# Kernel tuning notes

Measured on AMD Instinct MI355X. Metric: run time of the kernel, lower is better.

## Reference

```python
import jax, jax.numpy as jnp
import numpy as np

N, E, D, G, NTYPES = 50000, 400000, 64, 512, 64


def _bn(x, g, b):
    # BatchNorm1d in training mode: biased batch stats, eps=1e-5, affine g/b
    mu = x.mean(0)
    var = ((x - mu) ** 2).mean(0)
    return g * (x - mu) * jax.lax.rsqrt(var + 1e-5) + b


def _rotmat(a):
    t, p, q = a[0], a[1], a[2]
    ct, st = jnp.cos(t), jnp.sin(t)
    cp, sp = jnp.cos(p), jnp.sin(p)
    cq, sq = jnp.cos(q), jnp.sin(q)
    z = jnp.zeros(())
    o = jnp.ones(())
    Rt = jnp.array([[ct, -st, z], [st, ct, z], [z, z, o]])
    Rp = jnp.array([[cp, z, -sp], [z, o, z], [sp, z, cp]])
    Rq = jnp.array([[o, z, z], [z, cq, -sq], [z, sq, cq]])
    return Rt @ Rp @ Rq


def _egat(src, dst, nf, ef, Wnode, bnode, Wni, Wnj, Wfij, attn, H):
    # DGL EGATConv: edge feats from src/dst node + edge projections, edge-softmax attention over dst
    n = nf.shape[0]
    f_out = jax.nn.leaky_relu((nf @ Wni)[src] + (nf @ Wnj)[dst] + ef @ Wfij)  # [E, H*D]
    f_out = f_out.reshape(-1, H, D)
    e = (f_out * attn[None]).sum(-1)  # [E, H]
    emax = jax.ops.segment_max(e, dst, num_segments=n)
    ee = jnp.exp(e - emax[dst])
    a = ee / jax.ops.segment_sum(ee, dst, num_segments=n)[dst]
    hsrc = (nf @ Wnode + bnode).reshape(n, H, D)[src]
    h_out = jax.ops.segment_sum(hsrc * a[:, :, None], dst, num_segments=n)  # [N, H, D]
    return h_out, f_out


def _layer(src, dst, nh, eh, p, H, last):
    Wnode, bnode, Wni, Wnj, Wfij, attn, bnn_g, bnn_b, bne_g, bne_b, Wpn, bpn, Wpe, bpe = p
    hn, he = _egat(src, dst, nh, eh, Wnode, bnode, Wni, Wnj, Wfij, attn, H)
    if last:
        hn, he = hn.mean(1), he.mean(1)
    else:
        hn, he = hn.reshape(hn.shape[0], -1), he.reshape(he.shape[0], -1)
    hn = _bn(hn, bnn_g, bnn_b)
    he = _bn(he, bne_g, bne_b)
    return hn @ Wpn + bpn + nh, he @ Wpe + bpe + eh


def setup_inputs():
    key = jax.random.key(0)
    kit = iter(jax.random.split(key, 64))

    def rn(shape, s=0.05):
        return jax.random.normal(next(kit), shape, dtype=jnp.float32) * s

    inp = {}
    inp["ntype"] = jax.random.randint(next(kit), (N, 1), 0, NTYPES)
    inp["src"] = jax.random.randint(next(kit), (E,), 0, N)
    inp["dst"] = jax.random.randint(next(kit), (E,), 0, N)
    inp["graph_ids"] = jnp.sort(jax.random.randint(next(kit), (N,), 0, G))
    inp["angles_rot"] = rn((3,), 1.0)
    inp["angles_ref"] = rn((3,), 1.0)
    inp["efeats"] = rn((E, 3), 1.0)
    inp["emb_table"] = rn((NTYPES, D))
    inp["enc_W"] = rn((D, D)); inp["enc_b"] = jnp.zeros((D,))
    inp["ee_W1"] = rn((3, D)); inp["ee_b1"] = jnp.zeros((D,))
    inp["ee_W2"] = rn((D, D)); inp["ee_b2"] = jnp.zeros((D,))
    for nm in ["enc_bn1", "enc_bn2", "ee_bn1", "ee_bn2"]:
        inp[nm + "_g"] = jnp.ones((D,)); inp[nm + "_b"] = jnp.zeros((D,))
    for l, H in [(0, 2), (1, 1)]:
        p = "l%d_" % l
        inp[p + "Wnode"] = rn((D, H * D)); inp[p + "bnode"] = jnp.zeros((H * D,))
        inp[p + "Wni"] = rn((D, H * D)); inp[p + "Wnj"] = rn((D, H * D)); inp[p + "Wfij"] = rn((D, H * D))
        inp[p + "attn"] = rn((H, D))
        inp[p + "bnn_g"] = jnp.ones((H * D,)); inp[p + "bnn_b"] = jnp.zeros((H * D,))
        inp[p + "bne_g"] = jnp.ones((H * D,)); inp[p + "bne_b"] = jnp.zeros((H * D,))
        inp[p + "Wpn"] = rn((H * D, D)); inp[p + "bpn"] = jnp.zeros((D,))
        inp[p + "Wpe"] = rn((H * D, D)); inp[p + "bpe"] = jnp.zeros((D,))
    inp["dec_W"] = rn((4, D, D)); inp["dec_b"] = jnp.zeros((4, D))
    inp["dec_bn_g"] = jnp.ones((4, D)); inp["dec_bn_b"] = jnp.zeros((4, D))
    inp["dec_prelu"] = jnp.full((4,), 0.25, dtype=jnp.float32)
    inp["dec_Wout"] = rn((D, 1)); inp["dec_bout"] = jnp.zeros((1,))
    return inp


def reference(efeats, emb_table, enc_bn1_g, enc_bn1_b, enc_W, enc_b, enc_bn2_g, enc_bn2_b, ee_W1, ee_b1, ee_bn1_g, ee_bn1_b, ee_W2, ee_b2, ee_bn2_g, ee_bn2_b, l0_Wnode, l0_bnode, l0_Wni, l0_Wnj, l0_Wfij, l0_attn, l0_bnn_g, l0_bnn_b, l0_bne_g, l0_bne_b, l0_Wpn, l0_bpn, l0_Wpe, l0_bpe, l1_Wnode, l1_bnode, l1_Wni, l1_Wnj, l1_Wfij, l1_attn, l1_bnn_g, l1_bnn_b, l1_bne_g, l1_bne_b, l1_Wpn, l1_bpn, l1_Wpe, l1_bpe, dec_W, dec_b, dec_bn_g, dec_bn_b, dec_prelu, dec_Wout, dec_bout, ntype, src, dst, graph_ids, angles_rot, angles_ref):
    # node encoder: Embedding -> BN -> ReLU -> Linear -> BN -> ReLU
    nh = emb_table[ntype[:, 0]]
    nh = jax.nn.relu(_bn(nh, enc_bn1_g, enc_bn1_b))
    nh = jax.nn.relu(_bn(nh @ enc_W + enc_b, enc_bn2_g, enc_bn2_b))

    def edge_enc(f):
        h = jax.nn.relu(_bn(f @ ee_W1 + ee_b1, ee_bn1_g, ee_bn1_b))
        return jax.nn.relu(_bn(h @ ee_W2 + ee_b2, ee_bn2_g, ee_bn2_b))

    # rotation matrices built from sampled angles; torch.tensor([...]) detaches -> stop_gradient
    R_rot = jax.lax.stop_gradient(_rotmat(angles_rot))
    R_ref = -jax.lax.stop_gradient(_rotmat(angles_ref))
    eh = edge_enc(efeats @ R_rot) + edge_enc(efeats @ R_ref)

    p0 = (l0_Wnode, l0_bnode, l0_Wni, l0_Wnj, l0_Wfij, l0_attn, l0_bnn_g, l0_bnn_b, l0_bne_g, l0_bne_b, l0_Wpn, l0_bpn, l0_Wpe, l0_bpe)
    p1 = (l1_Wnode, l1_bnode, l1_Wni, l1_Wnj, l1_Wfij, l1_attn, l1_bnn_g, l1_bnn_b, l1_bne_g, l1_bne_b, l1_Wpn, l1_bpn, l1_Wpe, l1_bpe)
    nh, eh = _layer(src, dst, nh, eh, p0, 2, False)
    h1 = nh
    nh, eh = _layer(src, dst, nh, eh, p1, 1, True)
    h2 = nh

    h = nh
    for i in range(4):
        h = _bn(h @ dec_W[i] + dec_b[i], dec_bn_g[i], dec_bn_b[i])
        h = jnp.where(h >= 0.0, h, dec_prelu[i] * h)
    h = h @ dec_Wout + dec_bout
    # dgl.sum_nodes: per-graph sum over batched graphs
    return (h1, h2, jax.ops.segment_sum(h, graph_ids, num_segments=G))
```

## Files before the change

kernel.cpp:

```cpp
#include <hip/hip_runtime.h>
#include <math.h>

#define NN 50000
#define NE 400000
#define NG 512
#define EPS 1e-5f
#define NSLOT 256

typedef unsigned int u32;
typedef unsigned short u16;

typedef __attribute__((ext_vector_type(8))) short s16x8;
typedef __attribute__((ext_vector_type(4))) float f32x4;

__device__ __forceinline__ float b2f(u16 h) { return __uint_as_float(((u32)h) << 16); }
__device__ __forceinline__ u16 f2b(float f) {
    u32 x = __float_as_uint(f);
    u32 r = x + 0x7fffu + ((x >> 16) & 1u);
    return (u16)(r >> 16);
}
struct alignas(16) U16x8 { u16 s[8]; };
struct alignas(8) U16x4 { u16 s[4]; };
struct alignas(4) U16x2 { u16 s[2]; };

// ... 64 lines not shown
__global__ __launch_bounds__(256) void scan_part_kernel(const int* __restrict__ deg,
                                                        int* __restrict__ bsum, int n) {
    int i = blockIdx.x * 256 + threadIdx.x;
    int v = (i < n) ? deg[i] : 0;
#pragma unroll
    for (int off = 1; off < 64; off <<= 1) v += __shfl_xor(v, off, 64);
    __shared__ int ws[4];
    if ((threadIdx.x & 63) == 0) ws[threadIdx.x >> 6] = v;
    __syncthreads();
    if (threadIdx.x == 0) bsum[blockIdx.x] = ws[0] + ws[1] + ws[2] + ws[3];
}

__global__ __launch_bounds__(256) void scan_top_kernel(int* __restrict__ bsum, int nb,
                                                       int* __restrict__ rowptr, int n,
                                                       int total) {
    __shared__ int s[256];
    int tid = threadIdx.x;
    s[tid] = (tid < nb) ? bsum[tid] : 0;
    __syncthreads();
    for (int off = 1; off < 256; off <<= 1) {
        int v = (tid >= off) ? s[tid - off] : 0;
        __syncthreads();
        s[tid] += v;
        __syncthreads();
    }
    if (tid < nb) bsum[tid] = (tid == 0) ? 0 : s[tid - 1];
    if (tid == 0) rowptr[n] = total;
}

__global__ __launch_bounds__(256) void scan_fill_kernel(const int* __restrict__ deg,
                                                        const int* __restrict__ bsum,
                                                        int* __restrict__ rowptr,
                                                        int* __restrict__ curs, int n) {
    __shared__ int s[256];
    int tid = threadIdx.x;
    int i = blockIdx.x * 256 + tid;
    int v = (i < n) ? deg[i] : 0;
    s[tid] = v;
    __syncthreads();
    for (int off = 1; off < 256; off <<= 1) {
        int t = (tid >= off) ? s[tid - off] : 0;
        __syncthreads();
        s[tid] += t;
        __syncthreads();
    }
    if (i < n) {
        int excl = s[tid] - v + bsum[blockIdx.x];
        rowptr[i] = excl;
        curs[i] = excl;
    }
}

__global__ __launch_bounds__(256) void fill_kernel(const int* __restrict__ src,
                                                   const int* __restrict__ dst, int E,
                                                   int* __restrict__ curs,
                                                   int* __restrict__ epos,
                                                   int* __restrict__ esrc) {
    int e = blockIdx.x * 256 + threadIdx.x;
    if (e >= E) return;
    int pos = atomicAdd(&curs[dst[e]], 1);
    epos[e] = pos;
    esrc[pos] = src[e];
}

__global__ __launch_bounds__(256) void gather_emb_kernel(const int* __restrict__ ntype,
                                                         const float* __restrict__ emb,
                                                         u16* __restrict__ out, int n) {
    long i = (long)blockIdx.x * 256 + threadIdx.x;
    long e = i >> 3;
    if (e >= n) return;
    int c0 = (int)(i & 7) * 8;
    int t = ntype[e];
    float4 a = *(const float4*)&emb[(long)t * 64 + c0];
    float4 b = *(const float4*)&emb[(long)t * 64 + c0 + 4];
    U16x8 o;
    o.s[0] = f2b(a.x); o.s[1] = f2b(a.y); o.s[2] = f2b(a.z); o.s[3] = f2b(a.w);
    o.s[4] = f2b(b.x); o.s[5] = f2b(b.y); o.s[6] = f2b(b.z); o.s[7] = f2b(b.w);
    *(U16x8*)&out[e * 64 + c0] = o;
}

__global__ __launch_bounds__(256) void efstats_kernel(const float* __restrict__ ef, int E,
                                                      float* __restrict__ raw) {
    int tid = threadIdx.x;
    float a[9];
#pragma unroll
    for (int j = 0; j < 9; ++j) a[j] = 0.f;
    for (long e = (long)blockIdx.x * 256 + tid; e < E; e += (long)gridDim.x * 256) {
        float f0 = ef[e * 3 + 0], f1 = ef[e * 3 + 1], f2 = ef[e * 3 + 2];
        a[0] += f0; a[1] += f1; a[2] += f2;
        a[3] += f0 * f0; a[4] += f1 * f1; a[5] += f2 * f2;
        a[6] += f0 * f1; a[7] += f0 * f2; a[8] += f1 * f2;
    }
#pragma unroll
    for (int off = 1; off < 64; off <<= 1)
#pragma unroll
        for (int j = 0; j < 9; ++j) a[j] += __shfl_xor(a[j], off, 64);
    __shared__ float sred[4][9];
    int wv = tid >> 6, ln = tid & 63;
    if (ln == 0)
#pragma unroll
        for (int j = 0; j < 9; ++j) sred[wv][j] = a[j];
    __syncthreads();
    if (tid < 9) {
        float v = sred[0][tid] + sred[1][tid] + sred[2][tid] + sred[3][tid];
        atomicAdd(&raw[(size_t)(blockIdx.x & (NSLOT - 1)) * 16 + tid], v);
    }
}

__global__ void ee_stats_kernel(const float* __restrict__ efraw, const float* __restrict__ RWrot,
                                const float* __restrict__ RWref, const float* __restrict__ b1,
                                float* __restrict__ S_rot, float* __restrict__ S_ref, int E) {
    __shared__ float m[9];
    int t = threadIdx.x;
    if (t < 9) {
        float s = 0.f;
// ... 46 lines not shown
        if (tid < off) {
            f4add(sA[tid], sA[tid + off]); f4add(sB[tid], sB[tid + off]);
            f4add(sC[tid], sC[tid + off]); f4add(sD[tid], sD[tid + off]);
        }
        __syncthreads();
    }
    if (tid < TPR) {
        float* slot = raw + (size_t)(blockIdx.x & (NSLOT - 1)) * 256;
        int c = tid * 8;
        float4 a = sA[tid], b = sB[tid], cq = sC[tid], d = sD[tid];
        atomicAdd(&slot[c + 0], a.x); atomicAdd(&slot[c + 1], a.y);
        atomicAdd(&slot[c + 2], a.z); atomicAdd(&slot[c + 3], a.w);
        atomicAdd(&slot[c + 4], b.x); atomicAdd(&slot[c + 5], b.y);
        atomicAdd(&slot[c + 6], b.z); atomicAdd(&slot[c + 7], b.w);
        atomicAdd(&slot[COLS + c + 0], cq.x); atomicAdd(&slot[COLS + c + 1], cq.y);
        atomicAdd(&slot[COLS + c + 2], cq.z); atomicAdd(&slot[COLS + c + 3], cq.w);
        atomicAdd(&slot[COLS + c + 4], d.x); atomicAdd(&slot[COLS + c + 5], d.y);
        atomicAdd(&slot[COLS + c + 6], d.z); atomicAdd(&slot[COLS + c + 7], d.w);
    }
}

__global__ __launch_bounds__(256) void finalize_stats_kernel(const float* __restrict__ raw,
                                                             float* __restrict__ stats, int n) {
    int i = threadIdx.x;
    if (i >= n) return;
    float s = 0.f;
    for (int r = 0; r < NSLOT; ++r) s += raw[r * 256 + i];
    stats[i] = s;
}

__global__ __launch_bounds__(256) void bn_act_kernel(const u16* __restrict__ x,
                                                     u16* __restrict__ y, long rows, int cols,
                                                     const float* __restrict__ acc,
                                                     const float* __restrict__ g,
                                                     const float* __restrict__ b,
                                                     float inv_rows) {
    long i = (long)blockIdx.x * 256 + threadIdx.x;
    long total8 = rows * (long)cols / 8;
    if (i >= total8) return;
    long base = i * 8;
    int c0 = (int)(base % cols);
    U16x8 xv = *(const U16x8*)&x[base];
    U16x8 o;
#pragma unroll
    for (int j = 0; j < 8; ++j) {
        int c = c0 + j;
        float mu = acc[c] * inv_rows;
        float var = acc[cols + c] * inv_rows - mu * mu;
        float al = g[c] * rsqrtf(fmaxf(var, 0.f) + EPS);
        float be = b[c] - mu * al;
        o.s[j] = f2b(fmaxf(al * b2f(xv.s[j]) + be, 0.f));
    }
    *(U16x8*)&y[base] = o;
}

__global__ __launch_bounds__(256) void ee_merge_kernel(
    const u16* __restrict__ A, const u16* __restrict__ B, u16* __restrict__ EH,
    const float* __restrict__ Sa, const float* __restrict__ Sb, const float* __restrict__ g,
    const float* __restrict__ b, float inv_rows) {
    __shared__ float ala[64], bea[64], alb[64], beb[64];
    int tid = threadIdx.x;
    if (tid < 64) {
        float mu = Sa[tid] * inv_rows;
        float var = Sa[64 + tid] * inv_rows - mu * mu;
        float a = g[tid] * rsqrtf(fmaxf(var, 0.f) + EPS);
        ala[tid] = a; bea[tid] = b[tid] - mu * a;
        mu = Sb[tid] * inv_rows;
        var = Sb[64 + tid] * inv_rows - mu * mu;
        a = g[tid] * rsqrtf(fmaxf(var, 0.f) + EPS);
        alb[tid] = a; beb[tid] = b[tid] - mu * a;
    }
    __syncthreads();
    long i = (long)blockIdx.x * 256 + tid;
    if (i >= (long)NE * 8) return;
    long base = i * 8;
    int c0 = (int)(base & 63);
    U16x8 xa = *(const U16x8*)&A[base];
    U16x8 xb = *(const U16x8*)&B[base];
    U16x8 o;
#pragma unroll
    for (int j = 0; j < 8; ++j) {
        int c = c0 + j;
        float va = fmaxf(ala[c] * b2f(xa.s[j]) + bea[c], 0.f);
        float vb = fmaxf(alb[c] * b2f(xb.s[j]) + beb[c], 0.f);
        o.s[j] = f2b(va + vb);
    }
    *(U16x8*)&EH[base] = o;
}


template <int K, int COLS, bool XBF, bool RBF, bool OBF, bool SOUT>
__global__ __launch_bounds__(256) void mfma_mm_kernel(
    const void* __restrict__ Xv, const u16* __restrict__ WT, const float* __restrict__ bias,
    const void* __restrict__ resv, void* __restrict__ Yv, int rows, int preop,
    const float* __restrict__ stats, const float* __restrict__ g, const float* __restrict__ b,
    float inv_rows, const float* __restrict__ prelu, int prelu_idx, float* __restrict__ raw) {
    constexpr int NCT = COLS / 16;
    constexpr int NKK = K / 32;
    __shared__ float al[K], be[K];
    __shared__ float ssum[SOUT ? COLS : 1], ssq[SOUT ? COLS : 1];
    const int tid = threadIdx.x;
    if (preop) {
        for (int k = tid; k < K; k += 256) {
            float mu = stats[k] * inv_rows;
            float var = stats[K + k] * inv_rows - mu * mu;
            float a = g[k] * rsqrtf(fmaxf(var, 0.f) + EPS);
            al[k] = a;
            be[k] = b[k] - mu * a;
        }
    }
    if (SOUT) {
        for (int i = tid; i < COLS; i += 256) { ssum[i] = 0.f; ssq[i] = 0.f; }
    }
    __syncthreads();
    const int lane = tid & 63, wv = tid >> 6;
    const int q = lane >> 4, rr = lane & 15;
    const long r0 = ((long)blockIdx.x * 4 + wv) * 16;
    const bool act = r0 < rows;
    const float pa = (preop == 3) ? prelu[prelu_idx] : 0.f;
    s16x8 afr[NKK];
    if (act) {
#pragma unroll
        for (int kk = 0; kk < NKK; ++kk) {
            float v[8];
            if (XBF) {
                U16x8 t = *(const U16x8*)((const u16*)Xv + (r0 + rr) * K + kk * 32 + q * 8);
#pragma unroll
                for (int j = 0; j < 8; ++j) v[j] = b2f(t.s[j]);
            } else {
                const float* xp = (const float*)Xv + (r0 + rr) * K + kk * 32 + q * 8;
                float4 t0 = *(const float4*)xp;
                float4 t1 = *(const float4*)(xp + 4);
                v[0] = t0.x; v[1] = t0.y; v[2] = t0.z; v[3] = t0.w;
                v[4] = t1.x; v[5] = t1.y; v[6] = t1.z; v[7] = t1.w;
            }
            union { u16 u[8]; s16x8 s; } o;
#pragma unroll
            for (int j = 0; j < 8; ++j) {
                float xx = v[j];
                if (preop) {
// ... 48 lines not shown
        }
    }
}

template <int COLS, bool XBF>
__global__ __launch_bounds__(256) void mfma_mm3_kernel(
    const void* __restrict__ Xv, const u16* __restrict__ WT0, const u16* __restrict__ WT1,
    const u16* __restrict__ WT2, const float* __restrict__ bias2, u16* __restrict__ Y0,
    u16* __restrict__ Y1, u16* __restrict__ Y2, int rows) {
    constexpr int NCT = COLS / 16;
    const int tid = threadIdx.x;
    const int lane = tid & 63, wv = tid >> 6;
    const int q = lane >> 4, rr = lane & 15;
    const long r0 = ((long)blockIdx.x * 4 + wv) * 16;
    if (r0 >= rows) return;
    s16x8 afr[2];
#pragma unroll
    for (int kk = 0; kk < 2; ++kk) {
        if (XBF) {
            afr[kk] = *(const s16x8*)((const u16*)Xv + (r0 + rr) * 64 + kk * 32 + q * 8);
        } else {
            const float* xp = (const float*)Xv + (r0 + rr) * 64 + kk * 32 + q * 8;
            float4 t0 = *(const float4*)xp;
            float4 t1 = *(const float4*)(xp + 4);
            union { u16 u[8]; s16x8 s; } o;
            o.u[0] = f2b(t0.x); o.u[1] = f2b(t0.y); o.u[2] = f2b(t0.z); o.u[3] = f2b(t0.w);
            o.u[4] = f2b(t1.x); o.u[5] = f2b(t1.y); o.u[6] = f2b(t1.z); o.u[7] = f2b(t1.w);
            afr[kk] = o.s;
        }
    }
    const u16* wts[3] = {WT0, WT1, WT2};
    u16* ys[3] = {Y0, Y1, Y2};
#pragma unroll
    for (int m = 0; m < 3; ++m) {
#pragma unroll
        for (int ct = 0; ct < NCT; ++ct) {
            f32x4 acc = (f32x4){0.f, 0.f, 0.f, 0.f};
#pragma unroll
            for (int kk = 0; kk < 2; ++kk) {
                s16x8 bfr = *(const s16x8*)&wts[m][(size_t)(ct * 16 + rr) * 64 + kk * 32 + q * 8];
                acc = __builtin_amdgcn_mfma_f32_16x16x32_bf16(afr[kk], bfr, acc, 0, 0, 0);
            }
            int col = ct * 16 + rr;
            float bb = (m == 2) ? bias2[col] : 0.f;
#pragma unroll
            for (int r = 0; r < 4; ++r) {
                long orr = r0 + q * 4 + r;
                ys[m][orr * COLS + col] = f2b(acc[r] + bb);
            }
        }
    }
}

__global__ __launch_bounds__(256) void mfma_ee_kernel(
    const float* __restrict__ ef, const float* __restrict__ RW, const float* __restrict__ b1v,
    const u16* __restrict__ W2T, const float* __restrict__ b2, u16* __restrict__ T2, int E,
    const float* __restrict__ stats, const float* __restrict__ g, const float* __restrict__ b,
    float inv_rows, float* __restrict__ raw) {
    __shared__ float rws[192];
    __shared__ float al[64], be[64];
    __shared__ float ssum[64], ssq[64];
    const int tid = threadIdx.x;
    if (tid < 192) rws[tid] = RW[tid];
    if (tid < 64) {
        float mu = stats[tid] * inv_rows;
        float var = stats[64 + tid] * inv_rows - mu * mu;
        float a = g[tid] * rsqrtf(fmaxf(var, 0.f) + EPS);
        al[tid] = a;
        be[tid] = b[tid] - mu * a + a * b1v[tid];
        ssum[tid] = 0.f;
        ssq[tid] = 0.f;
    }
    __syncthreads();
    const int lane = tid & 63, wv = tid >> 6;
    const int q = lane >> 4, rr = lane & 15;
    const long r0 = ((long)blockIdx.x * 4 + wv) * 16;
    const long ar = r0 + rr;
    float e0 = ef[ar * 3], e1 = ef[ar * 3 + 1], e2 = ef[ar * 3 + 2];
    s16x8 afr[2];
#pragma unroll
    for (int kk = 0; kk < 2; ++kk) {
        union { u16 u[8]; s16x8 v; } t;
#pragma unroll
        for (int j = 0; j < 8; ++j) {
            int k = kk * 32 + q * 8 + j;
            float tv = e0 * rws[k] + e1 * rws[64 + k] + e2 * rws[128 + k];
            t.u[j] = f2b(fmaxf(al[k] * tv + be[k], 0.f));
        }
        afr[kk] = t.v;
    }
    f32x4 acc[4];
#pragma unroll
    for (int ct = 0; ct < 4; ++ct) {
        acc[ct] = (f32x4){0.f, 0.f, 0.f, 0.f};
#pragma unroll
        for (int kk = 0; kk < 2; ++kk) {
            s16x8 bfr = *(const s16x8*)&W2T[(size_t)(ct * 16 + rr) * 64 + kk * 32 + q * 8];
            acc[ct] = __builtin_amdgcn_mfma_f32_16x16x32_bf16(afr[kk], bfr, acc[ct], 0, 0, 0);
        }
    }
#pragma unroll
    for (int ct = 0; ct < 4; ++ct) {
        int col = ct * 16 + rr;
        float bb = b2[col];
        float s = 0.f, qq = 0.f;
#pragma unroll
        for (int r = 0; r < 4; ++r) {
            long orr = r0 + q * 4 + r;
            float v = acc[ct][r] + bb;
            T2[orr * 64 + col] = f2b(v);
            s += v;
            qq += v * v;
        }
        s += __shfl_xor(s, 16, 64); s += __shfl_xor(s, 32, 64);
        qq += __shfl_xor(qq, 16, 64); qq += __shfl_xor(qq, 32, 64);
        if (q == 0) {
            atomicAdd(&ssum[col], s);
            atomicAdd(&ssq[col], qq);
        }
    }
    __syncthreads();
    if (tid < 64) {
        float* slot = raw + (size_t)(blockIdx.x & (NSLOT - 1)) * 256;
        atomicAdd(&slot[tid], ssum[tid]);
        atomicAdd(&slot[64 + tid], ssq[tid]);
    }
}

template <int COLS, bool WRITE_F, bool SOUT>
__global__ __launch_bounds__(256) void mfma_egat_kernel(
    const u16* __restrict__ EH, const u16* __restrict__ WT, const u16* __restrict__ NI,
    const u16* __restrict__ NJ, const int* __restrict__ src, const int* __restrict__ dst,
    const int* __restrict__ epos, const float* __restrict__ attn, u16* __restrict__ Fout,
    float* __restrict__ eatt, int E, float* __restrict__ raw) {
    constexpr int H = COLS / 64;
    constexpr int NCT = COLS / 16;
    constexpr int FSTR = COLS + 8;
    __shared__ float ssum[SOUT ? COLS : 1];
    __shared__ float ssq[SOUT ? COLS : 1];
    __shared__ u16 fts[WRITE_F ? 64 * FSTR : 1];
    const int tid = threadIdx.x;
    if (SOUT) {
        for (int i = tid; i < COLS; i += 256) { ssum[i] = 0.f; ssq[i] = 0.f; }
        __syncthreads();
    }
    const int lane = tid & 63, wv = tid >> 6;
    const int q = lane >> 4, rr = lane & 15;
    const long r0 = ((long)blockIdx.x * 4 + wv) * 16;
    s16x8 afr[2];
#pragma unroll
    for (int kk = 0; kk < 2; ++kk)
        afr[kk] = *(const s16x8*)&EH[(r0 + rr) * 64 + kk * 32 + q * 8];
    int sidx[4], didx[4];
#pragma unroll
    for (int r = 0; r < 4; ++r) {
        long orr = r0 + q * 4 + r;
        sidx[r] = src[orr];
        didx[r] = dst[orr];
    }
    f32x4 acc[NCT];
#pragma unroll
    for (int ct = 0; ct < NCT; ++ct) {
        acc[ct] = (f32x4){0.f, 0.f, 0.f, 0.f};
#pragma unroll
        for (int kk = 0; kk < 2; ++kk) {
            s16x8 bfr = *(const s16x8*)&WT[(size_t)(ct * 16 + rr) * 64 + kk * 32 + q * 8];
            acc[ct] = __builtin_amdgcn_mfma_f32_16x16x32_bf16(afr[kk], bfr, acc[ct], 0, 0, 0);
        }
    }
    float part[H][4];
#pragma unroll
    for (int h = 0; h < H; ++h)
#pragma unroll
        for (int r = 0; r < 4; ++r) part[h][r] = 0.f;
#pragma unroll
    for (int ct = 0; ct < NCT; ++ct) {
        int col = ct * 16 + rr;
        float av = attn[col];
        const int h = (H == 2) ? (ct >> 2) : 0;
        float fs = 0.f, fq = 0.f;
#pragma unroll
        for (int r = 0; r < 4; ++r) {
            float f = acc[ct][r] + b2f(NI[(size_t)sidx[r] * COLS + col]) +
                      b2f(NJ[(size_t)didx[r] * COLS + col]);
            f = (f >= 0.f) ? f : 0.01f * f;
            if (WRITE_F) fts[(wv * 16 + q * 4 + r) * FSTR + col] = f2b(f);
            part[h][r] += f * av;
            if (SOUT) { fs += f; fq += f * f; }
        }
        if (SOUT) {
            fs += __shfl_xor(fs, 16, 64); fs += __shfl_xor(fs, 32, 64);
            fq += __shfl_xor(fq, 16, 64); fq += __shfl_xor(fq, 32, 64);
            if (q == 0) {
                atomicAdd(&ssum[col], fs);
                atomicAdd(&ssq[col], fq);
            }
        }
    }
#pragma unroll
    for (int h = 0; h < H; ++h)
#pragma unroll
        for (int r = 0; r < 4; ++r) {
            float p = part[h][r];
            p += __shfl_xor(p, 1, 64);
            p += __shfl_xor(p, 2, 64);
            p += __shfl_xor(p, 4, 64);
            p += __shfl_xor(p, 8, 64);
            part[h][r] = p;
        }
    if (rr == 0) {
#pragma unroll
        for (int r = 0; r < 4; ++r) {
            long pos = epos[r0 + q * 4 + r];
            if (H == 2) {
                eatt[pos * 2 + 0] = part[0][r];
                eatt[pos * 2 + 1] = part[1][r];
            } else {
                eatt[pos] = part[0][r];
            }
        }
    }
    if (WRITE_F) {
        __syncthreads();
        const long rb = (long)blockIdx.x * 64;
        constexpr int CH = COLS / 8;
        for (int i = tid; i < 64 * CH; i += 256) {
            int row = i / CH, c8 = i % CH;
            U16x8 v = *(const U16x8*)&fts[row * FSTR + c8 * 8];
            *(U16x8*)&Fout[(rb + row) * COLS + c8 * 8] = v;
        }
    }
    if (SOUT) {
        __syncthreads();
        float* slot = raw + (size_t)(blockIdx.x & (NSLOT - 1)) * 256;
        for (int i = tid; i < COLS; i += 256) {
            atomicAdd(&slot[i], ssum[i]);
            atomicAdd(&slot[COLS + i], ssq[i]);
        }
    }
}

__global__ __launch_bounds__(256) void mfma_pe_kernel(
    const u16* __restrict__ X, const u16* __restrict__ WT, const float* __restrict__ bias,
    u16* __restrict__ EHio, int E, const float* __restrict__ stats, const float* __restrict__ g,
    const float* __restrict__ b, float inv_rows) {
    __shared__ float al[128], be[128];
    const int tid = threadIdx.x;
    if (tid < 128) {
        float mu = stats[tid] * inv_rows;
        float var = stats[128 + tid] * inv_rows - mu * mu;
        float a = g[tid] * rsqrtf(fmaxf(var, 0.f) + EPS);
        al[tid] = a;
        be[tid] = b[tid] - mu * a;
    }
    __syncthreads();
    const int lane = tid & 63, wv = tid >> 6;
    const int q = lane >> 4, rr = lane & 15;
    const long r0 = ((long)blockIdx.x * 4 + wv) * 16;
    s16x8 afr[4];
#pragma unroll
    for (int kk = 0; kk < 4; ++kk) {
        U16x8 t = *(const U16x8*)&X[(r0 + rr) * 128 + kk * 32 + q * 8];
        union { u16 u[8]; s16x8 v; } o;
#pragma unroll
        for (int j = 0; j < 8; ++j) {
            int k = kk * 32 + q * 8 + j;
            o.u[j] = f2b(al[k] * b2f(t.s[j]) + be[k]);
        }
        afr[kk] = o.v;
    }
    f32x4 acc[4];
#pragma unroll
    for (int ct = 0; ct < 4; ++ct) {
        acc[ct] = (f32x4){0.f, 0.f, 0.f, 0.f};
#pragma unroll
        for (int kk = 0; kk < 4; ++kk) {
            s16x8 bfr = *(const s16x8*)&WT[(size_t)(ct * 16 + rr) * 128 + kk * 32 + q * 8];
            acc[ct] = __builtin_amdgcn_mfma_f32_16x16x32_bf16(afr[kk], bfr, acc[ct], 0, 0, 0);
        }
    }
#pragma unroll
    for (int ct = 0; ct < 4; ++ct) {
        int col = ct * 16 + rr;
        float bb = bias[col];
#pragma unroll
        for (int r = 0; r < 4; ++r) {
            long orr = r0 + q * 4 + r;
            float v = acc[ct][r] + bb + b2f(EHio[orr * 64 + col]);
            EHio[orr * 64 + col] = f2b(v);
        }
    }
}

template <int COLS, bool SOUT>
__global__ __launch_bounds__(256) void csr_aggregate_kernel(
    const int* __restrict__ rowptr, const int* __restrict__ esrc,
    const float* __restrict__ eatt, const u16* __restrict__ nodeh, float* __restrict__ hout,
    int n, float* __restrict__ raw) {
    constexpr int H = COLS / 64;
    constexpr int TPN = COLS / 2;
    constexpr int NPB = 256 / TPN;
    __shared__ float ssum[SOUT ? COLS : 1];
    __shared__ float ssq[SOUT ? COLS : 1];
    int tid = threadIdx.x;
    if (SOUT) {
        for (int i = tid; i < COLS; i += 256) { ssum[i] = 0.f; ssq[i] = 0.f; }
        __syncthreads();
    }
    int node = blockIdx.x * NPB + tid / TPN;
    bool act = node < n;
    int c = (tid % TPN) * 2;
    float a0 = 0.f, a1 = 0.f;
    if (act) {
        int h = (H == 2) ? (c >> 6) : 0;
        int p0 = rowptr[node], p1 = rowptr[node + 1];
        float m = -INFINITY, s = 0.f;
        for (int p = p0; p < p1; ++p) {
            float v = eatt[(long)p * H + h];
            float mn = fmaxf(m, v);
            s = s * expf(m - mn) + expf(v - mn);
            m = mn;
        }
        float inv = (s > 0.f) ? 1.f / s : 0.f;
        for (int p = p0; p < p1; ++p) {
            float w = expf(eatt[(long)p * H + h] - m) * inv;
            U16x2 v = *(const U16x2*)&nodeh[(long)esrc[p] * COLS + c];
            a0 += b2f(v.s[0]) * w;
            a1 += b2f(v.s[1]) * w;
        }
        *(float2*)&hout[(long)node * COLS + c] = make_float2(a0, a1);
    }
    if (SOUT) {
        if (act) {
            atomicAdd(&ssum[c], a0);
            atomicAdd(&ssum[c + 1], a1);
            atomicAdd(&ssq[c], a0 * a0);
            atomicAdd(&ssq[c + 1], a1 * a1);
        }
        __syncthreads();
        float* slot = raw + (size_t)(blockIdx.x & (NSLOT - 1)) * 256;
        for (int i = tid; i < COLS; i += 256) {
// ... 56 lines not shown
    const float* l0_Wnj = (const float*)d_in[25];
    const float* l0_Wfij = (const float*)d_in[26];
    const float* l0_attn = (const float*)d_in[27];
    const float* l0_bnn_g = (const float*)d_in[28];
    const float* l0_bnn_b = (const float*)d_in[29];
    const float* l0_bne_g = (const float*)d_in[30];
    const float* l0_bne_b = (const float*)d_in[31];
    const float* l0_Wpn = (const float*)d_in[32];
    const float* l0_bpn = (const float*)d_in[33];
    const float* l0_Wpe = (const float*)d_in[34];
    const float* l0_bpe = (const float*)d_in[35];
    const float* l1_Wnode = (const float*)d_in[36];
    const float* l1_bnode = (const float*)d_in[37];
    const float* l1_Wni = (const float*)d_in[38];
    const float* l1_Wnj = (const float*)d_in[39];
    const float* l1_Wfij = (const float*)d_in[40];
    const float* l1_attn = (const float*)d_in[41];
    const float* l1_bnn_g = (const float*)d_in[42];
    const float* l1_bnn_b = (const float*)d_in[43];
    const float* l1_Wpn = (const float*)d_in[46];
    const float* l1_bpn = (const float*)d_in[47];
    const float* dec_W = (const float*)d_in[50];
    const float* dec_b = (const float*)d_in[51];
    const float* dec_bn_g = (const float*)d_in[52];
    const float* dec_bn_b = (const float*)d_in[53];
    const float* dec_prelu = (const float*)d_in[54];
    const float* dec_Wout = (const float*)d_in[55];
    const float* dec_bout = (const float*)d_in[56];

    float* out = (float*)d_out;
    float* H1 = out;
    float* H2 = out + (long)NN * 64;
    float* POOL = out + (long)NN * 128;

    char* base = (char*)d_ws;
    size_t off = 0;
    auto alloc = [&](size_t bytes) -> void* {
        off = (off + 255) & ~(size_t)255;
        void* p = base + off;
        off += bytes;
        return p;
    };
    u16* EH = (u16*)alloc((size_t)NE * 64 * 2);
    u16* F128 = (u16*)alloc((size_t)NE * 128 * 2);
    float* EATT = (float*)alloc((size_t)NE * 2 * 4);
    u16* NX = (u16*)alloc((size_t)NN * 64 * 2);
    u16* NI = (u16*)alloc((size_t)NN * 128 * 2);
    u16* NJ = (u16*)alloc((size_t)NN * 128 * 2);
    u16* NHH = (u16*)alloc((size_t)NN * 128 * 2);
    float* HOUT0 = (float*)alloc((size_t)NN * 128 * 4);
    float* HOUT1 = (float*)alloc((size_t)NN * 64 * 4);
    int* ROWPTR = (int*)alloc((size_t)(NN + 1) * 4);
    int* CURS = (int*)alloc((size_t)NN * 4);
    int* EPOS = (int*)alloc((size_t)NE * 4);
    int* ESRC = (int*)alloc((size_t)NE * 4);
    int* BSUM = (int*)alloc((size_t)256 * 4);
    float* RWrot = (float*)alloc(256 * 4);
    float* RWref = (float*)alloc(256 * 4);
    u16* EncWT = (u16*)alloc(4096 * 2);
    u16* W2T = (u16*)alloc(4096 * 2);
    u16* Wni0T = (u16*)alloc(8192 * 2);
    u16* Wnj0T = (u16*)alloc(8192 * 2);
    u16* Wnd0T = (u16*)alloc(8192 * 2);
    u16* WfijT0 = (u16*)alloc(8192 * 2);
    u16* Wpn0T = (u16*)alloc(8192 * 2);
    u16* WpeT = (u16*)alloc(8192 * 2);
    u16* Wni1T = (u16*)alloc(4096 * 2);
    u16* Wnj1T = (u16*)alloc(4096 * 2);
    u16* Wnd1T = (u16*)alloc(4096 * 2);
    u16* WfijT1 = (u16*)alloc(4096 * 2);
    u16* Wpn1T = (u16*)alloc(4096 * 2);
    u16* DecT0 = (u16*)alloc(4096 * 2);
    u16* DecT1 = (u16*)alloc(4096 * 2);
    u16* DecT2 = (u16*)alloc(4096 * 2);
    u16* DecT3 = (u16*)alloc(4096 * 2);
    float* STATS = (float*)alloc((size_t)13 * 256 * 4);
    char* zstart = base + ((off + 255) & ~(size_t)255);
    int* DEG = (int*)alloc((size_t)NN * 4);
    float* STATS_RAW = (float*)alloc((size_t)13 * NSLOT * 256 * 4);
    float* RAWEF = (float*)alloc((size_t)NSLOT * 16 * 4);
    char* zend = base + off;
    if (ws_size < off) return;

    u16* T2a = F128;
    u16* T2b = F128 + (size_t)NE * 64;
    u16* NX0 = F128;
    u16* NT = F128 + (size_t)NE * 64;
    u16* DT0 = NI;
    u16* DT1 = NJ;

    auto RAW = [&](int idx) { return STATS_RAW + (size_t)idx * NSLOT * 256; };
    float* S_enc1 = STATS + 0 * 256;
    float* S_enc2 = STATS + 1 * 256;
    float* S_ee2r = STATS + 3 * 256;
    float* S_ee1r = STATS + 2 * 256;
    float* S_ee1f = STATS + 4 * 256;
    float* S_ee2f = STATS + 5 * 256;
    float* S_bnn0 = STATS + 6 * 256;
    float* S_bne0 = STATS + 7 * 256;
    float* S_bnn1 = STATS + 8 * 256;
    float* S_d0 = STATS + 9 * 256;
    float* S_d1 = STATS + 10 * 256;
    float* S_d2 = STATS + 11 * 256;
    float* S_d3 = STATS + 12 * 256;

    const float invN = 1.f / (float)NN;
    const float invE = 1.f / (float)NE;
    const int GS = 640;
    const int MFB = NE / 64;
    const int NNB = (NN + 63) / 64;
    const int NB = (NN + 255) / 256;

    hipMemsetAsync(zstart, 0, (size_t)(zend - zstart), stream);
    hipMemsetAsync(POOL, 0, (size_t)NG * 4, stream);

    setup_kernel<<<1, 64, 0, stream>>>(ang_rot, ang_ref, ee_W1, RWrot, RWref);
    {
        WtJobs j;
        const float* Ws[NWT] = {enc_W,  ee_W2,  l0_Wni, l0_Wnj, l0_Wnode, l0_Wfij,
                                l0_Wpn, l0_Wpe, l1_Wni, l1_Wnj, l1_Wnode, l1_Wfij,
                                l1_Wpn, dec_W,  dec_W + 4096, dec_W + 8192, dec_W + 12288};
        u16* Ts[NWT] = {EncWT, W2T, Wni0T, Wnj0T, Wnd0T, WfijT0, Wpn0T, WpeT, Wni1T,
                        Wnj1T, Wnd1T, WfijT1, Wpn1T, DecT0, DecT1, DecT2, DecT3};
        int Ks[NWT] = {64, 64, 64, 64, 64, 64, 128, 128, 64, 64, 64, 64, 64, 64, 64, 64, 64};
        int Cs[NWT] = {64, 64, 128, 128, 128, 128, 64, 64, 64, 64, 64, 64, 64, 64, 64, 64, 64};
        for (int i = 0; i < NWT; ++i) { j.W[i] = Ws[i]; j.WT[i] = Ts[i]; j.K[i] = Ks[i]; j.C[i] = Cs[i]; }
        wt_all_kernel<<<NWT * 32, 256, 0, stream>>>(j);
    }

    hist_kernel<<<(NE + 255) / 256, 256, 0, stream>>>(dst, NE, DEG);
    scan_part_kernel<<<NB, 256, 0, stream>>>(DEG, BSUM, NN);
    scan_top_kernel<<<1, 256, 0, stream>>>(BSUM, NB, ROWPTR, NN, NE);
    scan_fill_kernel<<<NB, 256, 0, stream>>>(DEG, BSUM, ROWPTR, CURS, NN);
    fill_kernel<<<(NE + 255) / 256, 256, 0, stream>>>(src, dst, NE, CURS, EPOS, ESRC);

    gather_emb_kernel<<<(NN * 8 + 255) / 256, 256, 0, stream>>>(ntype, emb, NX0, NN);
    colstats_kernel<64><<<GS, 256, 0, stream>>>(NX0, NN, RAW(0));
    finalize_stats_kernel<<<1, 256, 0, stream>>>(RAW(0), S_enc1, 128);
    mfma_mm_kernel<64, 64, true, false, true, true><<<NNB, 256, 0, stream>>>(
        NX0, EncWT, enc_b, nullptr, NT, NN, 2, S_enc1, enc_bn1_g, enc_bn1_b, invN, nullptr, 0,
        RAW(1));
    finalize_stats_kernel<<<1, 256, 0, stream>>>(RAW(1), S_enc2, 128);
    bn_act_kernel<<<(NN * 8 + 255) / 256, 256, 0, stream>>>(NT, NX, NN, 64, S_enc2, enc_bn2_g,
                                                            enc_bn2_b, invN);

    efstats_kernel<<<256, 256, 0, stream>>>(efeats, NE, RAWEF);
    ee_stats_kernel<<<1, 128, 0, stream>>>(RAWEF, RWrot, RWref, ee_b1, S_ee1r, S_ee1f, NE);
    mfma_ee_kernel<<<MFB, 256, 0, stream>>>(efeats, RWrot, ee_b1, W2T, ee_b2, T2a, NE, S_ee1r,
                                            ee_bn1_g, ee_bn1_b, invE, RAW(3));
    mfma_ee_kernel<<<MFB, 256, 0, stream>>>(efeats, RWref, ee_b1, W2T, ee_b2, T2b, NE, S_ee1f,
                                            ee_bn1_g, ee_bn1_b, invE, RAW(5));
    finalize_stats_kernel<<<1, 256, 0, stream>>>(RAW(3), S_ee2r, 128);
    finalize_stats_kernel<<<1, 256, 0, stream>>>(RAW(5), S_ee2f, 128);
    ee_merge_kernel<<<(int)(((long)NE * 8 + 255) / 256), 256, 0, stream>>>(
        T2a, T2b, EH, S_ee2r, S_ee2f, ee_bn2_g, ee_bn2_b, invE);

    mfma_mm3_kernel<128, true><<<NNB, 256, 0, stream>>>(NX, Wni0T, Wnj0T, Wnd0T, l0_bnode, NI,
                                                        NJ, NHH, NN);
    mfma_egat_kernel<128, true, true><<<MFB, 256, 0, stream>>>(
        EH, WfijT0, NI, NJ, src, dst, EPOS, l0_attn, F128, EATT, NE, RAW(7));
    finalize_stats_kernel<<<1, 256, 0, stream>>>(RAW(7), S_bne0, 256);
    csr_aggregate_kernel<128, true><<<(NN + 3) / 4, 256, 0, stream>>>(ROWPTR, ESRC, EATT, NHH,
                                                                      HOUT0, NN, RAW(6));
    finalize_stats_kernel<<<1, 256, 0, stream>>>(RAW(6), S_bnn0, 256);
    mfma_mm_kernel<128, 64, false, true, false, false><<<NNB, 256, 0, stream>>>(
        HOUT0, Wpn0T, l0_bpn, NX, H1, NN, 1, S_bnn0, l0_bnn_g, l0_bnn_b, invN, nullptr, 0,
        nullptr);
    mfma_pe_kernel<<<MFB, 256, 0, stream>>>(F128, WpeT, l0_bpe, EH, NE, S_bne0, l0_bne_g,
                                            l0_bne_b, invE);

    mfma_mm3_kernel<64, false><<<NNB, 256, 0, stream>>>(H1, Wni1T, Wnj1T, Wnd1T, l1_bnode, NI,
                                                        NJ, NHH, NN);
    mfma_egat_kernel<64, false, false><<<MFB, 256, 0, stream>>>(
        EH, WfijT1, NI, NJ, src, dst, EPOS, l1_attn, nullptr, EATT, NE, nullptr);
    csr_aggregate_kernel<64, true><<<(NN + 7) / 8, 256, 0, stream>>>(ROWPTR, ESRC, EATT, NHH,
                                                                     HOUT1, NN, RAW(8));
    finalize_stats_kernel<<<1, 256, 0, stream>>>(RAW(8), S_bnn1, 128);
    mfma_mm_kernel<64, 64, false, false, false, false><<<NNB, 256, 0, stream>>>(
        HOUT1, Wpn1T, l1_bpn, H1, H2, NN, 1, S_bnn1, l1_bnn_g, l1_bnn_b, invN, nullptr, 0,
        nullptr);

    mfma_mm_kernel<64, 64, false, false, true, true><<<NNB, 256, 0, stream>>>(
        H2, DecT0, dec_b, nullptr, DT0, NN, 0, nullptr, nullptr, nullptr, 0.f, nullptr, 0,
        RAW(9));
    finalize_stats_kernel<<<1, 256, 0, stream>>>(RAW(9), S_d0, 128);
    mfma_mm_kernel<64, 64, true, false, true, true><<<NNB, 256, 0, stream>>>(
        DT0, DecT1, dec_b + 64, nullptr, DT1, NN, 3, S_d0, dec_bn_g, dec_bn_b, invN, dec_prelu,
        0, RAW(10));
    finalize_stats_kernel<<<1, 256, 0, stream>>>(RAW(10), S_d1, 128);
    mfma_mm_kernel<64, 64, true, false, true, true><<<NNB, 256, 0, stream>>>(
        DT1, DecT2, dec_b + 128, nullptr, DT0, NN, 3, S_d1, dec_bn_g + 64, dec_bn_b + 64, invN,
        dec_prelu, 1, RAW(11));
    finalize_stats_kernel<<<1, 256, 0, stream>>>(RAW(11), S_d2, 128);
    mfma_mm_kernel<64, 64, true, false, true, true><<<NNB, 256, 0, stream>>>(
        DT0, DecT3, dec_b + 192, nullptr, DT1, NN, 3, S_d2, dec_bn_g + 128, dec_bn_b + 128,
        invN, dec_prelu, 2, RAW(12));
    finalize_stats_kernel<<<1, 256, 0, stream>>>(RAW(12), S_d3, 128);
    decoder_out_kernel<<<(NN + 3) / 4, 256, 0, stream>>>(DT1, S_d3, dec_bn_g + 192,
                                                         dec_bn_b + 192, dec_prelu, dec_Wout,
                                                         dec_bout, gid, POOL, NN, invN);
}
```

Before: 864.2 us.

## Permute edges into CSR order and recompute fused edge encoder instead of storing intermediates

Edges are permuted into destination-sorted order at CSR build time, with dst indices and edge features copied into that order, so all edge-level kernels run in CSR order and the epos scatter indirection goes away. The two edge-encoder branches are merged into one kernel that runs twice. The first pass only gathers BN statistics. The second pass recomputes both branches, applies BN2+ReLU, sums them and writes EH directly, which removes the two large bf16 intermediates and the separate merge kernel. The cost is redoing the small first-layer MFMA work, plus extra scattered writes in fill_kernel; the permuted order may also change gather locality for NI/NJ.

```diff
diff --git a/kernel.cpp b/kernel.cpp
--- a/kernel.cpp
+++ b/kernel.cpp
@@ -140,15 +140,21 @@
 }
 
 __global__ __launch_bounds__(256) void fill_kernel(const int* __restrict__ src,
-                                                   const int* __restrict__ dst, int E,
+                                                   const int* __restrict__ dst,
+                                                   const float* __restrict__ ef, int E,
                                                    int* __restrict__ curs,
-                                                   int* __restrict__ epos,
-                                                   int* __restrict__ esrc) {
+                                                   int* __restrict__ esrc,
+                                                   int* __restrict__ dsts,
+                                                   float* __restrict__ efp) {
     int e = blockIdx.x * 256 + threadIdx.x;
     if (e >= E) return;
-    int pos = atomicAdd(&curs[dst[e]], 1);
-    epos[e] = pos;
+    int d = dst[e];
+    int pos = atomicAdd(&curs[d], 1);
     esrc[pos] = src[e];
+    dsts[pos] = d;
+    efp[(long)pos * 3 + 0] = ef[(long)e * 3 + 0];
+    efp[(long)pos * 3 + 1] = ef[(long)e * 3 + 1];
+    efp[(long)pos * 3 + 2] = ef[(long)e * 3 + 2];
 }
 
 __global__ __launch_bounds__(256) void gather_emb_kernel(const int* __restrict__ ntype,
@@ -301,40 +307,6 @@
         o.s[j] = f2b(fmaxf(al * b2f(xv.s[j]) + be, 0.f));
     }
     *(U16x8*)&y[base] = o;
-}
-
-__global__ __launch_bounds__(256) void ee_merge_kernel(
-    const u16* __restrict__ A, const u16* __restrict__ B, u16* __restrict__ EH,
-    const float* __restrict__ Sa, const float* __restrict__ Sb, const float* __restrict__ g,
-    const float* __restrict__ b, float inv_rows) {
-    __shared__ float ala[64], bea[64], alb[64], beb[64];
-    int tid = threadIdx.x;
-    if (tid < 64) {
-        float mu = Sa[tid] * inv_rows;
-        float var = Sa[64 + tid] * inv_rows - mu * mu;
-        float a = g[tid] * rsqrtf(fmaxf(var, 0.f) + EPS);
-        ala[tid] = a; bea[tid] = b[tid] - mu * a;
-        mu = Sb[tid] * inv_rows;
-        var = Sb[64 + tid] * inv_rows - mu * mu;
-        a = g[tid] * rsqrtf(fmaxf(var, 0.f) + EPS);
-        alb[tid] = a; beb[tid] = b[tid] - mu * a;
-    }
-    __syncthreads();
-    long i = (long)blockIdx.x * 256 + tid;
-    if (i >= (long)NE * 8) return;
-    long base = i * 8;
-    int c0 = (int)(base & 63);
-    U16x8 xa = *(const U16x8*)&A[base];
-    U16x8 xb = *(const U16x8*)&B[base];
-    U16x8 o;
-#pragma unroll
-    for (int j = 0; j < 8; ++j) {
-        int c = c0 + j;
-        float va = fmaxf(ala[c] * b2f(xa.s[j]) + bea[c], 0.f);
-        float vb = fmaxf(alb[c] * b2f(xb.s[j]) + beb[c], 0.f);
-        o.s[j] = f2b(va + vb);
-    }
-    *(U16x8*)&EH[base] = o;
 }
 
 
@@ -489,87 +461,128 @@
     }
 }
 
-__global__ __launch_bounds__(256) void mfma_ee_kernel(
-    const float* __restrict__ ef, const float* __restrict__ RW, const float* __restrict__ b1v,
-    const u16* __restrict__ W2T, const float* __restrict__ b2, u16* __restrict__ T2, int E,
-    const float* __restrict__ stats, const float* __restrict__ g, const float* __restrict__ b,
-    float inv_rows, float* __restrict__ raw) {
-    __shared__ float rws[192];
-    __shared__ float al[64], be[64];
-    __shared__ float ssum[64], ssq[64];
+template <bool STORE>
+__global__ __launch_bounds__(256) void mfma_ee2_kernel(
+    const float* __restrict__ efp, const float* __restrict__ RWrot,
+    const float* __restrict__ RWref, const float* __restrict__ b1v, const u16* __restrict__ W2T,
+    const float* __restrict__ b2, const float* __restrict__ S1r, const float* __restrict__ S1f,
+    const float* __restrict__ S2r, const float* __restrict__ S2f, const float* __restrict__ g1,
+    const float* __restrict__ bn1b, const float* __restrict__ g2, const float* __restrict__ bn2b,
+    u16* __restrict__ EH, int E, float inv_rows, float* __restrict__ rawA,
+    float* __restrict__ rawB) {
+    constexpr int ESTR = 72;
+    __shared__ float rws[2][192];
+    __shared__ float al1[2][64], be1[2][64];
+    __shared__ float al2[2][64], be2[2][64];
+    __shared__ float ssum[2][64], ssq[2][64];
+    __shared__ u16 ets[STORE ? 64 * ESTR : 1];
     const int tid = threadIdx.x;
-    if (tid < 192) rws[tid] = RW[tid];
-    if (tid < 64) {
-        float mu = stats[tid] * inv_rows;
-        float var = stats[64 + tid] * inv_rows - mu * mu;
-        float a = g[tid] * rsqrtf(fmaxf(var, 0.f) + EPS);
-        al[tid] = a;
-        be[tid] = b[tid] - mu * a + a * b1v[tid];
-        ssum[tid] = 0.f;
-        ssq[tid] = 0.f;
+    if (tid < 192) {
+        rws[0][tid] = RWrot[tid];
+        rws[1][tid] = RWref[tid];
+    }
+    if (tid < 128) {
+        int br = tid >> 6, k = tid & 63;
+        const float* S1 = br ? S1f : S1r;
+        float mu = S1[k] * inv_rows;
+        float var = S1[64 + k] * inv_rows - mu * mu;
+        float a = g1[k] * rsqrtf(fmaxf(var, 0.f) + EPS);
+        al1[br][k] = a;
+        be1[br][k] = bn1b[k] - mu * a + a * b1v[k];
+        if (STORE) {
+            const float* S2 = br ? S2f : S2r;
+            mu = S2[k] * inv_rows;
+            var = S2[64 + k] * inv_rows - mu * mu;
+            a = g2[k] * rsqrtf(fmaxf(var, 0.f) + EPS);
+            al2[br][k] = a;
+            be2[br][k] = bn2b[k] - mu * a + a * b2[k];
+        } else {
+            ssum[br][k] = 0.f;
+            ssq[br][k] = 0.f;
+        }
     }
     __syncthreads();
     const int lane = tid & 63, wv = tid >> 6;
     const int q = lane >> 4, rr = lane & 15;
     const long r0 = ((long)blockIdx.x * 4 + wv) * 16;
     const long ar = r0 + rr;
-    float e0 = ef[ar * 3], e1 = ef[ar * 3 + 1], e2 = ef[ar * 3 + 2];
-    s16x8 afr[2];
-#pragma unroll
-    for (int kk = 0; kk < 2; ++kk) {
-        union { u16 u[8]; s16x8 v; } t;
-#pragma unroll
-        for (int j = 0; j < 8; ++j) {
-            int k = kk * 32 + q * 8 + j;
-            float tv = e0 * rws[k] + e1 * rws[64 + k] + e2 * rws[128 + k];
-            t.u[j] = f2b(fmaxf(al[k] * tv + be[k], 0.f));
-        }
-        afr[kk] = t.v;
-    }
-    f32x4 acc[4];
-#pragma unroll
-    for (int ct = 0; ct < 4; ++ct) {
-        acc[ct] = (f32x4){0.f, 0.f, 0.f, 0.f};
+    float e0 = efp[ar * 3], e1 = efp[ar * 3 + 1], e2 = efp[ar * 3 + 2];
+    float v0[4][4];
+#pragma unroll
+    for (int br = 0; br < 2; ++br) {
+        s16x8 afr[2];
 #pragma unroll
         for (int kk = 0; kk < 2; ++kk) {
-            s16x8 bfr = *(const s16x8*)&W2T[(size_t)(ct * 16 + rr) * 64 + kk * 32 + q * 8];
-            acc[ct] = __builtin_amdgcn_mfma_f32_16x16x32_bf16(afr[kk], bfr, acc[ct], 0, 0, 0);
-        }
-    }
-#pragma unroll
-    for (int ct = 0; ct < 4; ++ct) {
-        int col = ct * 16 + rr;
-        float bb = b2[col];
-        float s = 0.f, qq = 0.f;
-#pragma unroll
-        for (int r = 0; r < 4; ++r) {
-            long orr = r0 + q * 4 + r;
-            float v = acc[ct][r] + bb;
-            T2[orr * 64 + col] = f2b(v);
-            s += v;
-            qq += v * v;
-        }
-        s += __shfl_xor(s, 16, 64); s += __shfl_xor(s, 32, 64);
-        qq += __shfl_xor(qq, 16, 64); qq += __shfl_xor(qq, 32, 64);
-        if (q == 0) {
-            atomicAdd(&ssum[col], s);
-            atomicAdd(&ssq[col], qq);
+            union { u16 u[8]; s16x8 v; } t;
+#pragma unroll
+            for (int j = 0; j < 8; ++j) {
+                int k = kk * 32 + q * 8 + j;
+                float tv = e0 * rws[br][k] + e1 * rws[br][64 + k] + e2 * rws[br][128 + k];
+                t.u[j] = f2b(fmaxf(al1[br][k] * tv + be1[br][k], 0.f));
+            }
+            afr[kk] = t.v;
+        }
+#pragma unroll
+        for (int ct = 0; ct < 4; ++ct) {
+            f32x4 acc = (f32x4){0.f, 0.f, 0.f, 0.f};
+#pragma unroll
+            for (int kk = 0; kk < 2; ++kk) {
+                s16x8 bfr = *(const s16x8*)&W2T[(size_t)(ct * 16 + rr) * 64 + kk * 32 + q * 8];
+                acc = __builtin_amdgcn_mfma_f32_16x16x32_bf16(afr[kk], bfr, acc, 0, 0, 0);
+            }
+            int col = ct * 16 + rr;
+            if (STORE) {
+#pragma unroll
+                for (int r = 0; r < 4; ++r) {
+                    float v = fmaxf(al2[br][col] * acc[r] + be2[br][col], 0.f);
+                    if (br == 0) {
+                        v0[ct][r] = v;
+                    } else {
+                        ets[(wv * 16 + q * 4 + r) * ESTR + col] = f2b(v0[ct][r] + v);
+                    }
+                }
+            } else {
+                float bb = b2[col];
+                float s = 0.f, qq = 0.f;
+#pragma unroll
+                for (int r = 0; r < 4; ++r) {
+                    float v = acc[r] + bb;
+                    s += v;
+                    qq += v * v;
+                }
+                s += __shfl_xor(s, 16, 64); s += __shfl_xor(s, 32, 64);
+                qq += __shfl_xor(qq, 16, 64); qq += __shfl_xor(qq, 32, 64);
+                if (q == 0) {
+                    atomicAdd(&ssum[br][col], s);
+                    atomicAdd(&ssq[br][col], qq);
+                }
+            }
         }
     }
     __syncthreads();
-    if (tid < 64) {
-        float* slot = raw + (size_t)(blockIdx.x & (NSLOT - 1)) * 256;
-        atomicAdd(&slot[tid], ssum[tid]);
-        atomicAdd(&slot[64 + tid], ssq[tid]);
+    if (STORE) {
+        const long rb = (long)blockIdx.x * 64;
+        for (int i = tid; i < 64 * 8; i += 256) {
+            int row = i >> 3, c8 = i & 7;
+            U16x8 v = *(const U16x8*)&ets[row * ESTR + c8 * 8];
+            *(U16x8*)&EH[(rb + row) * 64 + c8 * 8] = v;
+        }
+    } else {
+        if (tid < 128) {
+            int br = tid >> 6, k = tid & 63;
+            float* slot = (br ? rawB : rawA) + (size_t)(blockIdx.x & (NSLOT - 1)) * 256;
+            atomicAdd(&slot[k], ssum[br][k]);
+            atomicAdd(&slot[64 + k], ssq[br][k]);
+        }
     }
 }
 
 template <int COLS, bool WRITE_F, bool SOUT>
 __global__ __launch_bounds__(256) void mfma_egat_kernel(
     const u16* __restrict__ EH, const u16* __restrict__ WT, const u16* __restrict__ NI,
-    const u16* __restrict__ NJ, const int* __restrict__ src, const int* __restrict__ dst,
-    const int* __restrict__ epos, const float* __restrict__ attn, u16* __restrict__ Fout,
-    float* __restrict__ eatt, int E, float* __restrict__ raw) {
+    const u16* __restrict__ NJ, const int* __restrict__ srcs, const int* __restrict__ dsts,
+    const float* __restrict__ attn, u16* __restrict__ Fout, float* __restrict__ eatt, int E,
+    float* __restrict__ raw) {
     constexpr int H = COLS / 64;
     constexpr int NCT = COLS / 16;
     constexpr int FSTR = COLS + 8;
@@ -592,8 +605,8 @@
 #pragma unroll
     for (int r = 0; r < 4; ++r) {
         long orr = r0 + q * 4 + r;
-        sidx[r] = src[orr];
-        didx[r] = dst[orr];
+        sidx[r] = srcs[orr];
+        didx[r] = dsts[orr];
     }
     f32x4 acc[NCT];
 #pragma unroll
@@ -648,7 +661,7 @@
     if (rr == 0) {
 #pragma unroll
         for (int r = 0; r < 4; ++r) {
-            long pos = epos[r0 + q * 4 + r];
+            long pos = r0 + q * 4 + r;
             if (H == 2) {
                 eatt[pos * 2 + 0] = part[0][r];
                 eatt[pos * 2 + 1] = part[1][r];
@@ -706,24 +719,20 @@
         }
         afr[kk] = o.v;
     }
-    f32x4 acc[4];
 #pragma unroll
     for (int ct = 0; ct < 4; ++ct) {
-        acc[ct] = (f32x4){0.f, 0.f, 0.f, 0.f};
+        f32x4 acc = (f32x4){0.f, 0.f, 0.f, 0.f};
 #pragma unroll
         for (int kk = 0; kk < 4; ++kk) {
             s16x8 bfr = *(const s16x8*)&WT[(size_t)(ct * 16 + rr) * 128 + kk * 32 + q * 8];
-            acc[ct] = __builtin_amdgcn_mfma_f32_16x16x32_bf16(afr[kk], bfr, acc[ct], 0, 0, 0);
-        }
-    }
-#pragma unroll
-    for (int ct = 0; ct < 4; ++ct) {
+            acc = __builtin_amdgcn_mfma_f32_16x16x32_bf16(afr[kk], bfr, acc, 0, 0, 0);
+        }
         int col = ct * 16 + rr;
         float bb = bias[col];
 #pragma unroll
         for (int r = 0; r < 4; ++r) {
             long orr = r0 + q * 4 + r;
-            float v = acc[ct][r] + bb + b2f(EHio[orr * 64 + col]);
+            float v = acc[r] + bb + b2f(EHio[orr * 64 + col]);
             EHio[orr * 64 + col] = f2b(v);
         }
     }
@@ -886,8 +895,9 @@
     float* HOUT1 = (float*)alloc((size_t)NN * 64 * 4);
     int* ROWPTR = (int*)alloc((size_t)(NN + 1) * 4);
     int* CURS = (int*)alloc((size_t)NN * 4);
-    int* EPOS = (int*)alloc((size_t)NE * 4);
     int* ESRC = (int*)alloc((size_t)NE * 4);
+    int* DSTS = (int*)alloc((size_t)NE * 4);
+    float* EFP = (float*)alloc((size_t)NE * 3 * 4);
     int* BSUM = (int*)alloc((size_t)256 * 4);
     float* RWrot = (float*)alloc(256 * 4);
     float* RWref = (float*)alloc(256 * 4);
@@ -916,18 +926,16 @@
     char* zend = base + off;
     if (ws_size < off) return;
 
-    u16* T2a = F128;
-    u16* T2b = F128 + (size_t)NE * 64;
     u16* NX0 = F128;
-    u16* NT = F128 + (size_t)NE * 64;
+    u16* NT = F128 + (size_t)NN * 64;
     u16* DT0 = NI;
     u16* DT1 = NJ;
 
     auto RAW = [&](int idx) { return STATS_RAW + (size_t)idx * NSLOT * 256; };
     float* S_enc1 = STATS + 0 * 256;
     float* S_enc2 = STATS + 1 * 256;
+    float* S_ee1r = STATS + 2 * 256;
     float* S_ee2r = STATS + 3 * 256;
-    float* S_ee1r = STATS + 2 * 256;
     float* S_ee1f = STATS + 4 * 256;
     float* S_ee2f = STATS + 5 * 256;
     float* S_bnn0 = STATS + 6 * 256;
@@ -966,7 +974,8 @@
     scan_part_kernel<<<NB, 256, 0, stream>>>(DEG, BSUM, NN);
     scan_top_kernel<<<1, 256, 0, stream>>>(BSUM, NB, ROWPTR, NN, NE);
     scan_fill_kernel<<<NB, 256, 0, stream>>>(DEG, BSUM, ROWPTR, CURS, NN);
-    fill_kernel<<<(NE + 255) / 256, 256, 0, stream>>>(src, dst, NE, CURS, EPOS, ESRC);
+    fill_kernel<<<(NE + 255) / 256, 256, 0, stream>>>(src, dst, efeats, NE, CURS, ESRC, DSTS,
+                                                      EFP);
 
     gather_emb_kernel<<<(NN * 8 + 255) / 256, 256, 0, stream>>>(ntype, emb, NX0, NN);
     colstats_kernel<64><<<GS, 256, 0, stream>>>(NX0, NN, RAW(0));
@@ -980,19 +989,19 @@
 
     efstats_kernel<<<256, 256, 0, stream>>>(efeats, NE, RAWEF);
     ee_stats_kernel<<<1, 128, 0, stream>>>(RAWEF, RWrot, RWref, ee_b1, S_ee1r, S_ee1f, NE);
-    mfma_ee_kernel<<<MFB, 256, 0, stream>>>(efeats, RWrot, ee_b1, W2T, ee_b2, T2a, NE, S_ee1r,
-                                            ee_bn1_g, ee_bn1_b, invE, RAW(3));
-    mfma_ee_kernel<<<MFB, 256, 0, stream>>>(efeats, RWref, ee_b1, W2T, ee_b2, T2b, NE, S_ee1f,
-                                            ee_bn1_g, ee_bn1_b, invE, RAW(5));
+    mfma_ee2_kernel<false><<<MFB, 256, 0, stream>>>(
+        EFP, RWrot, RWref, ee_b1, W2T, ee_b2, S_ee1r, S_ee1f, nullptr, nullptr, ee_bn1_g,
+        ee_bn1_b, nullptr, nullptr, nullptr, NE, invE, RAW(3), RAW(5));
     finalize_stats_kernel<<<1, 256, 0, stream>>>(RAW(3), S_ee2r, 128);
     finalize_stats_kernel<<<1, 256, 0, stream>>>(RAW(5), S_ee2f, 128);
-    ee_merge_kernel<<<(int)(((long)NE * 8 + 255) / 256), 256, 0, stream>>>(
-        T2a, T2b, EH, S_ee2r, S_ee2f, ee_bn2_g, ee_bn2_b, invE);
+    mfma_ee2_kernel<true><<<MFB, 256, 0, stream>>>(
+        EFP, RWrot, RWref, ee_b1, W2T, ee_b2, S_ee1r, S_ee1f, S_ee2r, S_ee2f, ee_bn1_g, ee_bn1_b,
+        ee_bn2_g, ee_bn2_b, EH, NE, invE, nullptr, nullptr);
 
     mfma_mm3_kernel<128, true><<<NNB, 256, 0, stream>>>(NX, Wni0T, Wnj0T, Wnd0T, l0_bnode, NI,
                                                         NJ, NHH, NN);
     mfma_egat_kernel<128, true, true><<<MFB, 256, 0, stream>>>(
-        EH, WfijT0, NI, NJ, src, dst, EPOS, l0_attn, F128, EATT, NE, RAW(7));
+        EH, WfijT0, NI, NJ, ESRC, DSTS, l0_attn, F128, EATT, NE, RAW(7));
     finalize_stats_kernel<<<1, 256, 0, stream>>>(RAW(7), S_bne0, 256);
     csr_aggregate_kernel<128, true><<<(NN + 3) / 4, 256, 0, stream>>>(ROWPTR, ESRC, EATT, NHH,
                                                                       HOUT0, NN, RAW(6));
@@ -1006,7 +1015,7 @@
     mfma_mm3_kernel<64, false><<<NNB, 256, 0, stream>>>(H1, Wni1T, Wnj1T, Wnd1T, l1_bnode, NI,
                                                         NJ, NHH, NN);
     mfma_egat_kernel<64, false, false><<<MFB, 256, 0, stream>>>(
-        EH, WfijT1, NI, NJ, src, dst, EPOS, l1_attn, nullptr, EATT, NE, nullptr);
+        EH, WfijT1, NI, NJ, ESRC, DSTS, l1_attn, nullptr, EATT, NE, nullptr);
     csr_aggregate_kernel<64, true><<<(NN + 7) / 8, 256, 0, stream>>>(ROWPTR, ESRC, EATT, NHH,
                                                                      HOUT1, NN, RAW(8));
     finalize_stats_kernel<<<1, 256, 0, stream>>>(RAW(8), S_bnn1, 128);
```

New measurement: 878.0 us. No clear change (+1.6%).
